# Kernel tuning notes

Hardware: AMD Instinct MI355X
Metric: run time of the kernel (lower is better)

The kernel has to match this reference:

```python
import jax, jax.numpy as jnp
import numpy as np

# dims: T tokens, E experts, D model dim, F ffn dim, C per-expert capacity, K top-k routing
T, E, D, F, C, K = 4096, 8, 1024, 4096, 1536, 2


def setup_inputs() -> dict:
    key = jax.random.key(0)
    k_x, k_lg, k_w1, k_w2 = jax.random.split(key, 4)
    x = jax.random.normal(k_x, (T, D), jnp.float32)
    # external router: top-K of logits per token, softmax weights over kept logits
    logits = jax.random.normal(k_lg, (T, E), jnp.float32)
    topv, topi = jax.lax.top_k(logits, K)                      # (T,K)
    rows = jnp.arange(T)[:, None]
    route_mask = jnp.zeros((T, E), bool).at[rows, topi].set(True)
    route_weight = jnp.zeros((T, E), jnp.float32).at[rows, topi].set(
        jax.nn.softmax(topv, axis=-1))
    # stacked homogeneous expert MLP params (E leading axis, as in _stack_group)
    W1 = jax.random.normal(k_w1, (E, D, F), jnp.float32) / np.sqrt(D)
    b1 = jnp.zeros((E, F), jnp.float32)
    W2 = jax.random.normal(k_w2, (E, F, D), jnp.float32) / np.sqrt(F)
    b2 = jnp.zeros((E, D), jnp.float32)
    return dict(x=x, route_mask=route_mask, route_weight=route_weight,
                W1=W1, b1=b1, W2=W2, b2=b2)


def reference(x, route_mask, route_weight, W1, b1, W2, b2):
    """MoE with per-expert capacity: top-C tokens per expert by route weight,
    gather -> vmapped expert MLP -> weighted scatter-combine.
    Math identical to the one-hot slot einsums ('ect,t...->ec...' dispatch and
    'ecf,ect,te->tf' combine) of the original, expressed as gather/scatter.
    """
    Tn, En = route_mask.shape
    w_te = jnp.where(route_mask, route_weight, 0.0)            # (T,E)
    # per-expert scores; unrouted tokens get -inf so they can never be selected
    w_et = jnp.where(route_mask.T, w_te.T, -jnp.inf)           # (E,T)
    vals, idx = jax.lax.top_k(w_et, C)                         # (E,C) token ids per slot
    valid = jnp.isfinite(vals)                                  # slot actually filled
    # dispatch: gather token features into (E,C,D); empty slots are zero rows
    xe = x[idx] * valid[..., None]
    # grouped expert MLP (vmap over E via batched einsum)
    h = jax.nn.relu(jnp.einsum('ecd,edf->ecf', xe, W1) + b1[:, None, :])
    out = jnp.einsum('ecf,efd->ecd', h, W2) + b2[:, None, :]    # (E,C,D)
    # combine: y[t] = sum over slots assigned to t of w_te[t,e] * out[e,c]
    gain = jnp.where(valid, jnp.take_along_axis(w_te.T, idx, axis=1), 0.0)  # (E,C)
    y = jnp.zeros((Tn, out.shape[-1]), out.dtype)
    y = y.at[idx.reshape(-1)].add((out * gain[..., None]).reshape(-1, out.shape[-1]))
    return y
```

## Files before the change

kernel.cpp:

```cpp
#include <hip/hip_runtime.h>
#include <hip/hip_bf16.h>
#include <stdint.h>

#define T_TOK 4096
#define NE    8
#define DM    1024
#define FF    4096
#define CAP   1536

typedef __attribute__((ext_vector_type(8))) __bf16 bf16x8;
typedef __attribute__((ext_vector_type(4))) float  f32x4;

__device__ __forceinline__ void gload_lds16(const void* gptr, void* lptr) {
  __builtin_amdgcn_global_load_lds(
      (__attribute__((address_space(1))) void*)(uintptr_t)gptr,
      (__attribute__((address_space(3))) void*)(uintptr_t)lptr,
      16, 0, 0);
}


__global__ void conv_x_kernel(const float4* __restrict__ src, ushort4* __restrict__ dst, int n4) {
  int i = blockIdx.x * blockDim.x + threadIdx.x;
  if (i >= n4) return;
  float4 v = src[i];
  ushort4 o;
  o.x = __builtin_bit_cast(unsigned short, __float2bfloat16(v.x));
  o.y = __builtin_bit_cast(unsigned short, __float2bfloat16(v.y));
  o.z = __builtin_bit_cast(unsigned short, __float2bfloat16(v.z));
  o.w = __builtin_bit_cast(unsigned short, __float2bfloat16(v.w));
  dst[i] = o;
}

__global__ __launch_bounds__(256)
void tconv_kernel(const float* __restrict__ src, __hip_bfloat16* __restrict__ dst,
                  int R, int C) {
  __shared__ float tile[64][65];
  const int b  = blockIdx.z;
  const int r0 = blockIdx.y * 64;
  const int c0 = blockIdx.x * 64;
  const float* s = src + (size_t)b * R * C;
  __hip_bfloat16* d = dst + (size_t)b * R * C;
  const int tid = threadIdx.x;
  const int tx = tid & 63, ty = tid >> 6;
#pragma unroll
  for (int rr = ty; rr < 64; rr += 4)
    tile[rr][tx] = s[(size_t)(r0 + rr) * C + c0 + tx];
  __syncthreads();
  const int lg = tid & 15;
  const int cg = tid >> 4;
#pragma unroll
  for (int w = 0; w < 4; ++w) {
    const int cc = w * 16 + cg;
    const int r4 = lg * 4;
    ushort4 o;
    o.x = __builtin_bit_cast(unsigned short, __float2bfloat16(tile[r4 + 0][cc]));
    o.y = __builtin_bit_cast(unsigned short, __float2bfloat16(tile[r4 + 1][cc]));
    o.z = __builtin_bit_cast(unsigned short, __float2bfloat16(tile[r4 + 2][cc]));
    o.w = __builtin_bit_cast(unsigned short, __float2bfloat16(tile[r4 + 3][cc]));
    *(ushort4*)&d[(size_t)(c0 + cc) * R + r0 + r4] = o;
  }
}

__global__ void router_kernel(const float* __restrict__ rw, int* __restrict__ counts,
                              int* __restrict__ tok_ids, float* __restrict__ gains) {
  int t = blockIdx.x * blockDim.x + threadIdx.x;
  if (t >= T_TOK) return;
#pragma unroll
  for (int e = 0; e < NE; ++e) {
    float w = rw[t * NE + e];
    if (w > 0.f) {
      int pos = atomicAdd(&counts[e], 1);
      if (pos < CAP) {
        tok_ids[e * CAP + pos] = t;
        gains[e * CAP + pos]   = w;
      }
    }
  }
}

__global__ void pad_kernel(const int* __restrict__ counts, int* __restrict__ tok_ids,
                           float* __restrict__ gains) {
  int i = blockIdx.x * blockDim.x + threadIdx.x;
  if (i >= NE * CAP) return;
  int e = i / CAP, pos = i % CAP;
  int ne = min(counts[e], CAP);
  if (pos >= ne) { tok_ids[i] = 0; gains[i] = 0.f; }
}


template <int PASS>
__global__ __launch_bounds__(512, 2)
void moe_gemm8(const __hip_bfloat16* __restrict__ Asrc,
               const __hip_bfloat16* __restrict__ Bsrc,
               const float* __restrict__ bias,
               const int* __restrict__ counts,
               const int* __restrict__ tok_ids,
               const float* __restrict__ gains,
               __hip_bfloat16* __restrict__ Hout,
               float* __restrict__ y)
{
  constexpr int K   = (PASS == 1) ? DM : FF;
  constexpr int NP  = (PASS == 1) ? FF : DM;
  constexpr int MT  = CAP / 256;
  constexpr int NT  = NP / 256;
  constexpr int SK  = (PASS == 1) ? 1 : 2;
  constexpr int NWG = NE * MT * NT * SK;
  constexpr int KP  = K / SK;
  constexpr int KT  = KP / 64;
  constexpr int KTM = KT - 1;
  constexpr int NIT = KT / 2;

  const int id = (blockIdx.x & 7) * (NWG / 8) + (blockIdx.x >> 3);
  const int e  = id / (MT * NT * SK);
  int r        = id % (MT * NT * SK);
  const int sp = r / (MT * NT);
  r            = r % (MT * NT);
  const int nt = r / MT;
  const int mt = r % MT;

  const int Ne = min(counts[e], CAP);
  const int m0 = mt * 256;
  if (m0 >= Ne) return;
  const int n0 = nt * 256;
  const int k0 = sp * KP;

  __shared__ alignas(128) char LDSmem[131072];
  char* AsB = LDSmem;
  char* BsB = LDSmem + 65536;

  const int tid  = threadIdx.x;
  const int lane = tid & 63;
  const int wid  = tid >> 6;
  const int wm   = wid >> 2;
  const int wn   = wid & 3;
  const int fr   = lane & 15;
  const int fq   = lane >> 4;

  const int sr  = tid >> 3;
  const int kg  = tid & 7;
  const int ksw = ((kg ^ (sr & 7)) << 4);

  const char *aP[2][2], *bP[2][2];
#pragma unroll
  for (int h = 0; h < 2; ++h)
#pragma unroll
    for (int l = 0; l < 2; ++l) {
      const int row = h * 128 + l * 64 + sr;
      if (PASS == 1) {
        const int tok = tok_ids[e * CAP + m0 + row];
        aP[h][l] = (const char*)Asrc + ((size_t)tok * DM + k0) * 2 + ksw;
      } else {
        aP[h][l] = (const char*)Asrc + (((size_t)e * CAP + m0 + row) * FF + k0) * 2 + ksw;
      }
      bP[h][l] = (const char*)Bsrc + (((size_t)e * NP + n0 + row) * K + k0) * 2 + ksw;
    }

  const int kz0 = ((fq ^ (fr & 7)) << 4);
  const int kz1 = (((4 + fq) ^ (fr & 7)) << 4);
  const char* rdA0 = AsB + wm * 16384 + fr * 128 + kz0;
  const char* rdA1 = AsB + wm * 16384 + fr * 128 + kz1;
  const char* rdB0 = BsB + (wn >> 1) * 16384 + (wn & 1) * 8192 + fr * 128 + kz0;
  const char* rdB1 = BsB + (wn >> 1) * 16384 + (wn & 1) * 8192 + fr * 128 + kz1;

  f32x4  acc[8][4] = {};
  bf16x8 bfr[4][2], af[2][2];

#define STAGE_A(h, d, kt) do {                                                          \
    gload_lds16(aP[h][0] + (kt) * 128, AsB + (d) * 32768 + (h) * 16384 + tid * 16);     \
    gload_lds16(aP[h][1] + (kt) * 128, AsB + (d) * 32768 + (h) * 16384 + 8192 + tid * 16); \
  } while (0)
#define STAGE_B(h, d, kt) do {                                                          \
    gload_lds16(bP[h][0] + (kt) * 128, BsB + (d) * 32768 + (h) * 16384 + tid * 16);     \
    gload_lds16(bP[h][1] + (kt) * 128, BsB + (d) * 32768 + (h) * 16384 + 8192 + tid * 16); \
  } while (0)
#define VM4 asm volatile("s_waitcnt vmcnt(4)" ::: "memory")
#define PHASE(d, q, LOADB, STG, VM) do {                                                \
    if (LOADB) {                                                                        \
      _Pragma("unroll") for (int j = 0; j < 4; ++j) {                                   \
        bfr[j][0] = *(const bf16x8*)(rdB0 + (d) * 32768 + j * 2048);                    \
        bfr[j][1] = *(const bf16x8*)(rdB1 + (d) * 32768 + j * 2048);                    \
      }                                                                                 \
    }                                                                                   \
    af[0][0] = *(const bf16x8*)(rdA0 + (d) * 32768 + (q) * 4096);                       \
    af[0][1] = *(const bf16x8*)(rdA1 + (d) * 32768 + (q) * 4096);                       \
    af[1][0] = *(const bf16x8*)(rdA0 + (d) * 32768 + (q) * 4096 + 2048);                \
    af[1][1] = *(const bf16x8*)(rdA1 + (d) * 32768 + (q) * 4096 + 2048);                \
    STG;                                                                                \
    asm volatile("s_barrier" ::: "memory");                                             \
    asm volatile("s_waitcnt lgkmcnt(0)" ::: "memory");                                  \
    __builtin_amdgcn_sched_barrier(0);                                                  \
    __builtin_amdgcn_s_setprio(1);                                                      \
    _Pragma("unroll") for (int f = 0; f < 2; ++f)                                       \
      _Pragma("unroll") for (int j = 0; j < 4; ++j) {                                   \
        acc[(q) * 2 + f][j] = __builtin_amdgcn_mfma_f32_16x16x32_bf16(                  \
            af[f][0], bfr[j][0], acc[(q) * 2 + f][j], 0, 0, 0);                         \
        acc[(q) * 2 + f][j] = __builtin_amdgcn_mfma_f32_16x16x32_bf16(                  \
            af[f][1], bfr[j][1], acc[(q) * 2 + f][j], 0, 0, 0);                         \
      }                                                                                 \
    __builtin_amdgcn_s_setprio(0);                                                      \
    __builtin_amdgcn_sched_barrier(0);                                                  \
    VM;                                                                                 \
    asm volatile("s_barrier" ::: "memory");                                             \
  } while (0)

  STAGE_B(0, 0, 0); STAGE_B(1, 0, 0); STAGE_A(0, 0, 0); STAGE_A(1, 0, 0);
  STAGE_B(0, 1, 1); STAGE_B(1, 1, 1);
  asm volatile("s_waitcnt vmcnt(4)" ::: "memory");
  asm volatile("s_barrier" ::: "memory");

#pragma unroll 1
  for (int it = 0; it < NIT; ++it) {
    const int ta = 2 * it + 1;
    const int tb = (2 * it + 2) & KTM;
    const int tc = (2 * it + 3) & KTM;
    PHASE(0, 0, true,  STAGE_A(0, 1, ta), (void)0);
    PHASE(0, 1, false, STAGE_A(1, 1, ta), (void)0);
    PHASE(0, 2, false, STAGE_B(0, 0, tb), (void)0);
    PHASE(0, 3, false, STAGE_B(1, 0, tb), VM4);
    PHASE(1, 0, true,  STAGE_A(0, 0, tb), (void)0);
    PHASE(1, 1, false, STAGE_A(1, 0, tb), (void)0);
    PHASE(1, 2, false, STAGE_B(0, 1, tc), (void)0);
    PHASE(1, 3, false, STAGE_B(1, 1, tc), VM4);
  }
#undef STAGE_A
#undef STAGE_B
#undef VM4
#undef PHASE

  if (PASS == 1) {
#pragma unroll
    for (int nj = 0; nj < 4; ++nj) {
      const int col = n0 + wn * 64 + nj * 16 + fr;
      const float bv = bias[e * NP + col];
#pragma unroll
      for (int mi = 0; mi < 8; ++mi)
#pragma unroll
        for (int rr = 0; rr < 4; ++rr) {
          const int row = m0 + wm * 128 + mi * 16 + fq * 4 + rr;
          float v = acc[mi][nj][rr] + bv;
          Hout[((size_t)e * CAP + row) * FF + col] = __float2bfloat16(v > 0.f ? v : 0.f);
        }
    }
  } else {
    float bv[4];
#pragma unroll
    for (int nj = 0; nj < 4; ++nj)
      bv[nj] = (sp == 0) ? bias[e * NP + n0 + wn * 64 + nj * 16 + fr] : 0.f;
#pragma unroll
    for (int mi = 0; mi < 8; ++mi)
#pragma unroll
      for (int rr = 0; rr < 4; ++rr) {
        const int row  = m0 + wm * 128 + mi * 16 + fq * 4 + rr;
        const int slot = e * CAP + row;
        const float g  = gains[slot];
        if (g != 0.f) {
          const int tok = tok_ids[slot];
          float* yrow = y + (size_t)tok * DM + n0 + wn * 64 + fr;
#pragma unroll
          for (int nj = 0; nj < 4; ++nj)
            atomicAdd(yrow + nj * 16, (acc[mi][nj][rr] + bv[nj]) * g);
        }
      }
  }
}


extern "C" void kernel_launch(void* const* d_in, const int* in_sizes, int n_in,
                              void* d_out, int out_size, void* d_ws, size_t ws_size,
                              hipStream_t stream) {
  const float* x  = (const float*)d_in[0];
  const float* rw = (const float*)d_in[2];
  const float* W1 = (const float*)d_in[3];
  const float* b1 = (const float*)d_in[4];
  const float* W2 = (const float*)d_in[5];
  const float* b2 = (const float*)d_in[6];
  float* y = (float*)d_out;

  char* ws = (char*)d_ws;
  size_t off = 0;
  auto alloc = [&](size_t bytes) {
    void* p = ws + off;
    off = (off + bytes + 255) & ~(size_t)255;
    return p;
  };
  __hip_bfloat16* xb  = (__hip_bfloat16*)alloc((size_t)T_TOK * DM * 2);
  __hip_bfloat16* w1t = (__hip_bfloat16*)alloc((size_t)NE * DM * FF * 2);
  __hip_bfloat16* w2t = (__hip_bfloat16*)alloc((size_t)NE * FF * DM * 2);
  __hip_bfloat16* Hb  = (__hip_bfloat16*)alloc((size_t)NE * CAP * FF * 2);
  int*   counts  = (int*)alloc(NE * sizeof(int));
  int*   tok_ids = (int*)alloc((size_t)NE * CAP * sizeof(int));
  float* gains   = (float*)alloc((size_t)NE * CAP * sizeof(float));
  (void)ws_size; (void)in_sizes; (void)n_in; (void)out_size;

  hipMemsetAsync(y, 0, (size_t)T_TOK * DM * sizeof(float), stream);
  hipMemsetAsync(counts, 0, NE * sizeof(int), stream);

  conv_x_kernel<<<(T_TOK * DM / 4 + 255) / 256, 256, 0, stream>>>(
      (const float4*)x, (ushort4*)xb, T_TOK * DM / 4);
  tconv_kernel<<<dim3(FF / 64, DM / 64, NE), 256, 0, stream>>>(W1, w1t, DM, FF);
  tconv_kernel<<<dim3(DM / 64, FF / 64, NE), 256, 0, stream>>>(W2, w2t, FF, DM);
  router_kernel<<<(T_TOK + 255) / 256, 256, 0, stream>>>(rw, counts, tok_ids, gains);
  pad_kernel<<<(NE * CAP + 255) / 256, 256, 0, stream>>>(counts, tok_ids, gains);

  moe_gemm8<1><<<NE * (CAP / 256) * (FF / 256), 512, 0, stream>>>(
      xb, w1t, b1, counts, tok_ids, gains, Hb, nullptr);
  moe_gemm8<2><<<NE * (CAP / 256) * (DM / 256) * 2, 512, 0, stream>>>(
      Hb, w2t, b2, counts, tok_ids, gains, nullptr, y);
}
```

Before: 368.0 us.

## Replace 8-phase interleaved GEMM pipeline with simple double-buffered loop

The GEMM main loop drops its hand-scheduled 8-phase structure, which interleaved partial A/B tile loads with MFMA sub-blocks and a barrier per phase. It now uses a plain double buffer: prefetch the whole next K-tile, wait, then run all MFMAs on the current tile, with two barriers per K-tile. This cuts barrier count and simplifies scheduling. In exchange, each compute burst is coarser, load issue is less finely overlapped with MFMA work, and B fragments are re-read from LDS for each half-K step.

```diff
diff --git a/kernel.cpp b/kernel.cpp
--- a/kernel.cpp
+++ b/kernel.cpp
@@ -90,7 +90,7 @@
 
 template <int PASS>
 __global__ __launch_bounds__(512, 2)
-void moe_gemm8(const __hip_bfloat16* __restrict__ Asrc,
+void moe_gemm2(const __hip_bfloat16* __restrict__ Asrc,
                const __hip_bfloat16* __restrict__ Bsrc,
                const float* __restrict__ bias,
                const int* __restrict__ counts,
@@ -107,8 +107,6 @@
   constexpr int NWG = NE * MT * NT * SK;
   constexpr int KP  = K / SK;
   constexpr int KT  = KP / 64;
-  constexpr int KTM = KT - 1;
-  constexpr int NIT = KT / 2;
 
   const int id = (blockIdx.x & 7) * (NWG / 8) + (blockIdx.x >> 3);
   const int e  = id / (MT * NT * SK);
@@ -125,8 +123,6 @@
   const int k0 = sp * KP;
 
   __shared__ alignas(128) char LDSmem[131072];
-  char* AsB = LDSmem;
-  char* BsB = LDSmem + 65536;
 
   const int tid  = threadIdx.x;
   const int lane = tid & 63;
@@ -137,95 +133,72 @@
   const int fq   = lane >> 4;
 
   const int sr  = tid >> 3;
-  const int kg  = tid & 7;
-  const int ksw = ((kg ^ (sr & 7)) << 4);
-
-  const char *aP[2][2], *bP[2][2];
-#pragma unroll
-  for (int h = 0; h < 2; ++h)
-#pragma unroll
-    for (int l = 0; l < 2; ++l) {
-      const int row = h * 128 + l * 64 + sr;
-      if (PASS == 1) {
-        const int tok = tok_ids[e * CAP + m0 + row];
-        aP[h][l] = (const char*)Asrc + ((size_t)tok * DM + k0) * 2 + ksw;
-      } else {
-        aP[h][l] = (const char*)Asrc + (((size_t)e * CAP + m0 + row) * FF + k0) * 2 + ksw;
-      }
-      bP[h][l] = (const char*)Bsrc + (((size_t)e * NP + n0 + row) * K + k0) * 2 + ksw;
+  const int ksw = ((tid & 7) ^ (sr & 7)) << 4;
+
+  const char *aP[4], *bP[4];
+#pragma unroll
+  for (int i = 0; i < 4; ++i) {
+    const int row = i * 64 + sr;
+    if (PASS == 1) {
+      const int tok = tok_ids[e * CAP + m0 + row];
+      aP[i] = (const char*)Asrc + ((size_t)tok * DM + k0) * 2 + ksw;
+    } else {
+      aP[i] = (const char*)Asrc + (((size_t)e * CAP + m0 + row) * FF + k0) * 2 + ksw;
     }
-
-  const int kz0 = ((fq ^ (fr & 7)) << 4);
-  const int kz1 = (((4 + fq) ^ (fr & 7)) << 4);
-  const char* rdA0 = AsB + wm * 16384 + fr * 128 + kz0;
-  const char* rdA1 = AsB + wm * 16384 + fr * 128 + kz1;
-  const char* rdB0 = BsB + (wn >> 1) * 16384 + (wn & 1) * 8192 + fr * 128 + kz0;
-  const char* rdB1 = BsB + (wn >> 1) * 16384 + (wn & 1) * 8192 + fr * 128 + kz1;
-
-  f32x4  acc[8][4] = {};
-  bf16x8 bfr[4][2], af[2][2];
-
-#define STAGE_A(h, d, kt) do {                                                          \
-    gload_lds16(aP[h][0] + (kt) * 128, AsB + (d) * 32768 + (h) * 16384 + tid * 16);     \
-    gload_lds16(aP[h][1] + (kt) * 128, AsB + (d) * 32768 + (h) * 16384 + 8192 + tid * 16); \
+    bP[i] = (const char*)Bsrc + (((size_t)e * NP + n0 + row) * K + k0) * 2 + ksw;
+  }
+
+  const int kz0 = ((fq) ^ (fr & 7)) << 4;
+  const int kz1 = ((4 + fq) ^ (fr & 7)) << 4;
+  const char* rdA = LDSmem + wm * 16384 + fr * 128;
+  const char* rdB = LDSmem + 65536 + wn * 8192 + fr * 128;
+
+  f32x4 acc[8][4] = {};
+
+#define STAGE(d, kt) do {                                                       \
+    _Pragma("unroll") for (int i = 0; i < 4; ++i)                               \
+      gload_lds16(aP[i] + (kt) * 128, LDSmem + (d) * 32768 + i * 8192 + tid * 16); \
+    _Pragma("unroll") for (int i = 0; i < 4; ++i)                               \
+      gload_lds16(bP[i] + (kt) * 128, LDSmem + 65536 + (d) * 32768 + i * 8192 + tid * 16); \
   } while (0)
-#define STAGE_B(h, d, kt) do {                                                          \
-    gload_lds16(bP[h][0] + (kt) * 128, BsB + (d) * 32768 + (h) * 16384 + tid * 16);     \
-    gload_lds16(bP[h][1] + (kt) * 128, BsB + (d) * 32768 + (h) * 16384 + 8192 + tid * 16); \
+
+#define COMPUTE(d) do {                                                         \
+    __builtin_amdgcn_s_setprio(1);                                              \
+    _Pragma("unroll") for (int s = 0; s < 2; ++s) {                             \
+      const int kz = s ? kz1 : kz0;                                             \
+      bf16x8 bfr[4];                                                            \
+      _Pragma("unroll") for (int nj = 0; nj < 4; ++nj)                          \
+        bfr[nj] = *(const bf16x8*)(rdB + (d) * 32768 + nj * 2048 + kz);         \
+      _Pragma("unroll") for (int mi = 0; mi < 8; ++mi) {                        \
+        bf16x8 af = *(const bf16x8*)(rdA + (d) * 32768 + mi * 2048 + kz);       \
+        _Pragma("unroll") for (int nj = 0; nj < 4; ++nj)                        \
+          acc[mi][nj] = __builtin_amdgcn_mfma_f32_16x16x32_bf16(                \
+              af, bfr[nj], acc[mi][nj], 0, 0, 0);                               \
+      }                                                                         \
+    }                                                                           \
+    __builtin_amdgcn_s_setprio(0);                                              \
   } while (0)
-#define VM4 asm volatile("s_waitcnt vmcnt(4)" ::: "memory")
-#define PHASE(d, q, LOADB, STG, VM) do {                                                \
-    if (LOADB) {                                                                        \
-      _Pragma("unroll") for (int j = 0; j < 4; ++j) {                                   \
-        bfr[j][0] = *(const bf16x8*)(rdB0 + (d) * 32768 + j * 2048);                    \
-        bfr[j][1] = *(const bf16x8*)(rdB1 + (d) * 32768 + j * 2048);                    \
-      }                                                                                 \
-    }                                                                                   \
-    af[0][0] = *(const bf16x8*)(rdA0 + (d) * 32768 + (q) * 4096);                       \
-    af[0][1] = *(const bf16x8*)(rdA1 + (d) * 32768 + (q) * 4096);                       \
-    af[1][0] = *(const bf16x8*)(rdA0 + (d) * 32768 + (q) * 4096 + 2048);                \
-    af[1][1] = *(const bf16x8*)(rdA1 + (d) * 32768 + (q) * 4096 + 2048);                \
-    STG;                                                                                \
-    asm volatile("s_barrier" ::: "memory");                                             \
-    asm volatile("s_waitcnt lgkmcnt(0)" ::: "memory");                                  \
-    __builtin_amdgcn_sched_barrier(0);                                                  \
-    __builtin_amdgcn_s_setprio(1);                                                      \
-    _Pragma("unroll") for (int f = 0; f < 2; ++f)                                       \
-      _Pragma("unroll") for (int j = 0; j < 4; ++j) {                                   \
-        acc[(q) * 2 + f][j] = __builtin_amdgcn_mfma_f32_16x16x32_bf16(                  \
-            af[f][0], bfr[j][0], acc[(q) * 2 + f][j], 0, 0, 0);                         \
-        acc[(q) * 2 + f][j] = __builtin_amdgcn_mfma_f32_16x16x32_bf16(                  \
-            af[f][1], bfr[j][1], acc[(q) * 2 + f][j], 0, 0, 0);                         \
-      }                                                                                 \
-    __builtin_amdgcn_s_setprio(0);                                                      \
-    __builtin_amdgcn_sched_barrier(0);                                                  \
-    VM;                                                                                 \
-    asm volatile("s_barrier" ::: "memory");                                             \
-  } while (0)
-
-  STAGE_B(0, 0, 0); STAGE_B(1, 0, 0); STAGE_A(0, 0, 0); STAGE_A(1, 0, 0);
-  STAGE_B(0, 1, 1); STAGE_B(1, 1, 1);
-  asm volatile("s_waitcnt vmcnt(4)" ::: "memory");
-  asm volatile("s_barrier" ::: "memory");
-
+
+  STAGE(0, 0);
+  int cur = 0;
 #pragma unroll 1
-  for (int it = 0; it < NIT; ++it) {
-    const int ta = 2 * it + 1;
-    const int tb = (2 * it + 2) & KTM;
-    const int tc = (2 * it + 3) & KTM;
-    PHASE(0, 0, true,  STAGE_A(0, 1, ta), (void)0);
-    PHASE(0, 1, false, STAGE_A(1, 1, ta), (void)0);
-    PHASE(0, 2, false, STAGE_B(0, 0, tb), (void)0);
-    PHASE(0, 3, false, STAGE_B(1, 0, tb), VM4);
-    PHASE(1, 0, true,  STAGE_A(0, 0, tb), (void)0);
-    PHASE(1, 1, false, STAGE_A(1, 0, tb), (void)0);
-    PHASE(1, 2, false, STAGE_B(0, 1, tc), (void)0);
-    PHASE(1, 3, false, STAGE_B(1, 1, tc), VM4);
-  }
-#undef STAGE_A
-#undef STAGE_B
-#undef VM4
-#undef PHASE
+  for (int t = 0; t < KT - 1; ++t) {
+    STAGE(cur ^ 1, t + 1);
+    asm volatile("s_waitcnt vmcnt(8)" ::: "memory");
+    __builtin_amdgcn_s_barrier();
+    __builtin_amdgcn_sched_barrier(0);
+    COMPUTE(cur);
+    __builtin_amdgcn_sched_barrier(0);
+    __builtin_amdgcn_s_barrier();
+    cur ^= 1;
+  }
+  asm volatile("s_waitcnt vmcnt(0)" ::: "memory");
+  __builtin_amdgcn_s_barrier();
+  __builtin_amdgcn_sched_barrier(0);
+  COMPUTE(cur);
+
+#undef STAGE
+#undef COMPUTE
 
   if (PASS == 1) {
 #pragma unroll
@@ -302,8 +275,8 @@
   router_kernel<<<(T_TOK + 255) / 256, 256, 0, stream>>>(rw, counts, tok_ids, gains);
   pad_kernel<<<(NE * CAP + 255) / 256, 256, 0, stream>>>(counts, tok_ids, gains);
 
-  moe_gemm8<1><<<NE * (CAP / 256) * (FF / 256), 512, 0, stream>>>(
+  moe_gemm2<1><<<NE * (CAP / 256) * (FF / 256), 512, 0, stream>>>(
       xb, w1t, b1, counts, tok_ids, gains, Hb, nullptr);
-  moe_gemm8<2><<<NE * (CAP / 256) * (DM / 256) * 2, 512, 0, stream>>>(
+  moe_gemm2<2><<<NE * (CAP / 256) * (DM / 256) * 2, 512, 0, stream>>>(
       Hb, w2t, b2, counts, tok_ids, gains, nullptr, y);
 }
```

After: 385.9 us. 4.9% more time.
